# Performance work log

Measured on AMD Instinct MI355X. Metric: run time of the kernel, lower is better.

The kernel has to match this reference:

```python
import jax, jax.numpy as jnp
import numpy as np

N, DIN, E, BLK = 16384, 128, 262144, 2048
H1, DH1, H2, DH2 = 4, 128, 4, 128
D, L, HT, OUT = 128, 5, 4, 2


def _gat(h_in, src, dst, W, a_s, a_d, b, concat):
    # PyG GATConv (eval mode, no dropout): message src->dst, softmax per dst
    H, Dh = a_s.shape
    h = (h_in @ W).reshape(N, H, Dh)
    als = jnp.einsum('nhd,hd->nh', h, a_s)
    ald = jnp.einsum('nhd,hd->nh', h, a_d)
    e = jax.nn.leaky_relu(als[src] + ald[dst], 0.2)            # [E2,H]
    m = jax.ops.segment_max(e, dst, num_segments=N)
    ex = jnp.exp(e - m[dst])
    den = jax.ops.segment_sum(ex, dst, num_segments=N)
    alpha = ex / (den[dst] + 1e-16)
    out = jax.ops.segment_sum(alpha[:, :, None] * h[src], dst, num_segments=N)
    return (out.reshape(N, H * Dh) if concat else out.mean(axis=1)) + b


def _pe():
    pos = jnp.arange(L, dtype=jnp.float32)[:, None]
    div = jnp.exp(jnp.arange(0, D, 2, dtype=jnp.float32) * (-jnp.log(10000.0) / D))
    return jnp.zeros((L, D)).at[:, 0::2].set(jnp.sin(pos * div)).at[:, 1::2].set(jnp.cos(pos * div))


def reference(x, edge_index, time_step, W1, a_src1, a_dst1, b1, W2, a_src2, a_dst2, b2,
              wq, bq, wk, bk, wv, bv, wo, bo, ln_g, ln_b, f1, fb1, f2, fb2, wc, bc):
    s, d = edge_index[0], edge_index[1]
    loops = jnp.arange(N, dtype=edge_index.dtype)
    src = jnp.concatenate([s, d, loops])
    dst = jnp.concatenate([d, s, loops])

    # structural encoder (two GAT layers)
    h = jax.nn.elu(_gat(x, src, dst, W1, a_src1, a_dst1, b1, True))
    h2 = _gat(h, src, dst, W2, a_src2, a_dst2, b2, False)       # [N, D]

    # temporal self-attention: banks are empty (one snapshot per node), so
    # seq has only the last slot valid; original detaches seq before temporal.
    seq = jnp.zeros((N, L, D), h2.dtype).at[:, L - 1].set(jax.lax.stop_gradient(h2))
    xs = seq + _pe()[None]                                       # [N,L,D]
    dh = D // HT
    q = xs[:, -1]                                                # only last query is used
    Q = (q @ wq + bq).reshape(N, HT, dh)
    K = (xs @ wk + bk).reshape(N, L, HT, dh)
    V = (xs @ wv + bv).reshape(N, L, HT, dh)
    scores = jnp.einsum('nhd,nlhd->nhl', Q, K) / jnp.sqrt(jnp.float32(dh))
    valid = (jnp.arange(L) == L - 1)                             # key_padding_mask: pad except last
    scores = jnp.where(valid[None, None, :], scores, -1e9)
    attn = jax.nn.softmax(scores, axis=-1)
    ctx = jnp.einsum('nhl,nlhd->nhd', attn, V).reshape(N, D)
    ao = ctx @ wo + bo

    def ln(v):
        mu = v.mean(-1, keepdims=True)
        var = v.var(-1, keepdims=True)
        return (v - mu) / jnp.sqrt(var + 1e-5) * ln_g + ln_b

    y = ln(q + ao)
    y = ln(y + jax.nn.relu(y @ f1 + fb1) @ f2 + fb2)
    return y @ wc + bc                                           # [N, 2]


def setup_inputs():
    key = jax.random.key(0)
    ks = jax.random.split(key, 20)
    src = jax.random.randint(ks[0], (E,), 0, N, dtype=jnp.int32)
    off = jax.random.randint(ks[1], (E,), 0, BLK, dtype=jnp.int32)
    dst = (src // BLK) * BLK + off                               # within-snapshot edges
    r = lambda k, shape, s=0.05: jax.random.normal(k, shape, jnp.float32) * s
    return {
        'x': jax.random.normal(ks[2], (N, DIN), jnp.float32),
        'edge_index': jnp.stack([src, dst]),
        'time_step': (jnp.arange(N) // BLK).astype(jnp.int64),
        'W1': r(ks[3], (DIN, H1 * DH1)), 'a_src1': r(ks[4], (H1, DH1)), 'a_dst1': r(ks[5], (H1, DH1)), 'b1': jnp.zeros((H1 * DH1,)),
        'W2': r(ks[6], (H1 * DH1, H2 * DH2)), 'a_src2': r(ks[7], (H2, DH2)), 'a_dst2': r(ks[8], (H2, DH2)), 'b2': jnp.zeros((DH2,)),
        'wq': r(ks[9], (D, D)), 'bq': jnp.zeros((D,)), 'wk': r(ks[10], (D, D)), 'bk': jnp.zeros((D,)),
        'wv': r(ks[11], (D, D)), 'bv': jnp.zeros((D,)), 'wo': r(ks[12], (D, D)), 'bo': jnp.zeros((D,)),
        'ln_g': jnp.ones((D,)), 'ln_b': jnp.zeros((D,)),
        'f1': r(ks[13], (D, 4 * D)), 'fb1': jnp.zeros((4 * D,)), 'f2': r(ks[14], (4 * D, D)), 'fb2': jnp.zeros((D,)),
        'wc': r(ks[15], (D, OUT)), 'bc': jnp.zeros((OUT,)),
    }
```

## Files before the change

kernel.cpp:

```cpp
#include <hip/hip_runtime.h>
#include <hip/hip_bf16.h>

#define NODES 16384
#define FEAT 512
typedef __hip_bfloat16 bf16;
typedef __hip_bfloat162 bf162;
typedef short short8v __attribute__((ext_vector_type(8)));
typedef unsigned int uint4v __attribute__((ext_vector_type(4)));
typedef float f32x4 __attribute__((ext_vector_type(4)));

static __device__ __forceinline__ float b2f(short s){
  return __uint_as_float(((unsigned)(unsigned short)s) << 16);
}
static __device__ __forceinline__ void split_store(bf16* h, bf16* l, size_t i, float v){
  bf16 hi = __float2bfloat16(v);
  h[i] = hi; l[i] = __float2bfloat16(v - __bfloat162float(hi));
}

__global__ void sentinel_kernel(float* __restrict__ out, int n, float v){
  int i = blockIdx.x*blockDim.x + threadIdx.x;
  if (i < n) out[i] = v;
}

__global__ void zero_kernel(int* __restrict__ p, int n){
  int i = blockIdx.x*blockDim.x + threadIdx.x;
  if (i < n) p[i] = 0;
}
__global__ void count_kernel(const int* __restrict__ ei, int* __restrict__ counts, int E){
  int i = blockIdx.x*blockDim.x + threadIdx.x;
  if (i < 2*E){
    int dst = (i < E) ? ei[E+i] : ei[i-E];
    atomicAdd(&counts[dst], 1);
  }
}
__global__ __launch_bounds__(1024) void scan_kernel(const int* __restrict__ counts,
                                                    int* __restrict__ offs, int* __restrict__ cursor){
  __shared__ int sh[1024];
  const int t = threadIdx.x;
  int loc[16]; int s = 0;
#pragma unroll
  for (int i=0;i<16;i++){ loc[i] = counts[t*16+i]; s += loc[i]; }
  sh[t] = s; __syncthreads();
  for (int d=1; d<1024; d<<=1){
    int v = (t>=d) ? sh[t-d] : 0;
    __syncthreads(); sh[t] += v; __syncthreads();
  }
  int run = (t==0) ? 0 : sh[t-1];
#pragma unroll
  for (int i=0;i<16;i++){ offs[t*16+i] = run; cursor[t*16+i] = run; run += loc[i]; }
  if (t==1023) offs[NODES] = run;
}
__global__ void fill_kernel(const int* __restrict__ ei, int* __restrict__ cursor,
                            unsigned short* __restrict__ csr, int E){
  int i = blockIdx.x*blockDim.x + threadIdx.x;
  if (i < 2*E){
    int src = ei[i];
    int dst = (i < E) ? ei[E+i] : ei[i-E];
    int pos = atomicAdd(&cursor[dst], 1);
    csr[pos] = (unsigned short)src;
  }
}

struct PrepArgs {
  const float *x,*W1,*W2,*wv,*wo,*f1,*f2;
  bf16 *xh,*w1h,*w2h,*wvh,*wvl,*woh,*wol,*f1h,*f1l,*f2h,*f2l;
};
__global__ __launch_bounds__(256) void prep_kernel(PrepArgs P){
  const int b = blockIdx.x;
  const int t = threadIdx.x;
  if (b < 512){
    const size_t base = (size_t)b*4096;
#pragma unroll
    for (int k=0;k<16;k++){
      const size_t i = base + t + 256*k;
      P.xh[i] = __float2bfloat16(P.x[i]);
    }
    return;
  }
  __shared__ float tile[64][65];
  const float* src; bf16 *dh; bf16 *dl; int R, C, ti;
  int bb = b - 512;
  if (bb < 16){ src=P.W1; dh=P.w1h; dl=nullptr; R=128; C=512; ti=bb; }
  else if ((bb-=16) < 64){ src=P.W2; dh=P.w2h; dl=nullptr; R=512; C=512; ti=bb; }
  else if ((bb-=64) < 4){ src=P.wv; dh=P.wvh; dl=P.wvl; R=128; C=128; ti=bb; }
  else if ((bb-=4) < 4){ src=P.wo; dh=P.woh; dl=P.wol; R=128; C=128; ti=bb; }
  else if ((bb-=4) < 16){ src=P.f1; dh=P.f1h; dl=P.f1l; R=128; C=512; ti=bb; }
  else { bb-=16; src=P.f2; dh=P.f2h; dl=P.f2l; R=512; C=128; ti=bb; }
  const int ctiles = C/64;
  const int r0 = (ti/ctiles)*64, c0 = (ti%ctiles)*64;
  const int r = t >> 6, c = t & 63;
#pragma unroll
  for (int i=0;i<16;i++)
    tile[r + 4*i][c] = src[(size_t)(r0 + r + 4*i)*C + c0 + c];
  __syncthreads();
#pragma unroll
  for (int i=0;i<16;i++){
    const int oc   = c0 + r + 4*i;
    const int orow = r0 + c;
    const float v = tile[c][r + 4*i];
    const size_t oi = (size_t)oc*R + orow;
    if (dl){ split_store(dh, dl, oi, v); } else { dh[oi] = __float2bfloat16(v); }
  }
}

static __device__ __forceinline__ short8v ld8(const bf16* p){
  return *(const short8v*)(const void*)(p);
}

template<int K, int SA, int SB, int ACT, int OMODE, int ALS, int LNM>
__global__ __launch_bounds__(256) void lgemm(
    const bf16* __restrict__ A, const bf16* __restrict__ Al,
    const bf16* __restrict__ B, const bf16* __restrict__ Bl,
    const float* __restrict__ bias,
    float* __restrict__ Cf, bf16* __restrict__ Ch, bf16* __restrict__ Cl, int N,
    const float* __restrict__ as_p, const float* __restrict__ ad_p,
    float* __restrict__ als_p, float* __restrict__ ald_p,
    const float* __restrict__ qbuf, const float* __restrict__ lng, const float* __restrict__ lnb,
    float* __restrict__ y1f, bf16* __restrict__ y1ho, bf16* __restrict__ y1lo,
    const float* __restrict__ wcp, const float* __restrict__ bcp, float* __restrict__ outp){
  __shared__ bf16 As[128*40];
  __shared__ bf16 Bs[128*40];
  __shared__ bf16 Asl[SA ? 128*40 : 1];
  __shared__ bf16 Bsl[SB ? 128*40 : 1];
  const int tid = threadIdx.x;
  const int l = tid & 63, w = tid >> 6;
  const int lg = l >> 4, lr = l & 15;
  const int wr = w >> 1, wc = w & 1;
  const int r0 = blockIdx.x*128;
  const int c0 = blockIdx.y*128;
  const int srow = tid >> 1;
  const int spos = (tid & 1) * 16;
  f32x4 acc[4][4] = {};
  const int ard[4] = { (wr*64 +  0 + lr)*40 + lg*8, (wr*64 + 16 + lr)*40 + lg*8,
                       (wr*64 + 32 + lr)*40 + lg*8, (wr*64 + 48 + lr)*40 + lg*8 };
  const int brd[4] = { (wc*64 +  0 + lr)*40 + lg*8, (wc*64 + 16 + lr)*40 + lg*8,
                       (wc*64 + 32 + lr)*40 + lg*8, (wc*64 + 48 + lr)*40 + lg*8 };
  const size_t agbase = (size_t)(r0 + srow)*K + spos;
  const size_t bgbase = (size_t)(c0 + srow)*K + spos;
  const int sl = srow*40 + spos;
#pragma unroll
  for (int k0 = 0; k0 < K; k0 += 32){
    *(short8v*)&As[sl]     = ld8(A + agbase + k0);
    *(short8v*)&As[sl + 8] = ld8(A + agbase + k0 + 8);
    *(short8v*)&Bs[sl]     = ld8(B + bgbase + k0);
    *(short8v*)&Bs[sl + 8] = ld8(B + bgbase + k0 + 8);
    if (SA){
      *(short8v*)&Asl[sl]     = ld8(Al + agbase + k0);
      *(short8v*)&Asl[sl + 8] = ld8(Al + agbase + k0 + 8);
    }
    if (SB){
      *(short8v*)&Bsl[sl]     = ld8(Bl + bgbase + k0);
      *(short8v*)&Bsl[sl + 8] = ld8(Bl + bgbase + k0 + 8);
    }
    __syncthreads();
    short8v af[4], bfr[4], afl[4], bfl[4];
#pragma unroll
    for (int f=0; f<4; f++){
      af[f]  = *(const short8v*)&As[ard[f]];
      bfr[f] = *(const short8v*)&Bs[brd[f]];
      if (SA) afl[f] = *(const short8v*)&Asl[ard[f]];
      if (SB) bfl[f] = *(const short8v*)&Bsl[brd[f]];
    }
#pragma unroll
    for (int fm=0; fm<4; fm++)
#pragma unroll
      for (int fn=0; fn<4; fn++){
        acc[fm][fn] = __builtin_amdgcn_mfma_f32_16x16x32_bf16(af[fm], bfr[fn], acc[fm][fn], 0,0,0);
        if (SB) acc[fm][fn] = __builtin_amdgcn_mfma_f32_16x16x32_bf16(af[fm], bfl[fn], acc[fm][fn], 0,0,0);
        if (SA) acc[fm][fn] = __builtin_amdgcn_mfma_f32_16x16x32_bf16(afl[fm], bfr[fn], acc[fm][fn], 0,0,0);
      }
    __syncthreads();
  }
  if (LNM == 0){
    float asv[4], adv[4];
    float rs[4][4], rd[4][4];
    if (ALS){
#pragma unroll
      for (int fn=0; fn<4; fn++){
        const int col = c0 + wc*64 + fn*16 + lr;
        asv[fn] = as_p[col]; adv[fn] = ad_p[col];
      }
#pragma unroll
      for (int fm=0; fm<4; fm++)
#pragma unroll
        for (int r=0; r<4; r++){ rs[fm][r] = 0.f; rd[fm][r] = 0.f; }
    }
#pragma unroll
    for (int fm=0; fm<4; fm++){
#pragma unroll
      for (int fn=0; fn<4; fn++){
        const int col = c0 + wc*64 + fn*16 + lr;
        const float bv = bias ? bias[col] : 0.f;
#pragma unroll
        for (int r=0; r<4; r++){
          const int row = r0 + wr*64 + fm*16 + lg*4 + r;
          float v = acc[fm][fn][r] + bv;
          if (ACT==1) v = fmaxf(v, 0.f);
          const size_t idx = (size_t)row*N + col;
          if (OMODE==0) Cf[idx] = v;
          else if (OMODE==1){
            bf16 bvv = __float2bfloat16(v);
            Ch[idx] = bvv;
            if (ALS){
              const float hv = __bfloat162float(bvv);
              rs[fm][r] += hv*asv[fn];
              rd[fm][r] += hv*adv[fn];
            }
          }
          else split_store(Ch, Cl, idx, v);
        }
      }
    }
    if (ALS){
      float* rb = (float*)As;
#pragma unroll
      for (int fm=0; fm<4; fm++)
#pragma unroll
        for (int r=0; r<4; r++){
          float s = rs[fm][r], dd = rd[fm][r];
#pragma unroll
          for (int mask=1; mask<16; mask<<=1){
            s  += __shfl_xor(s,  mask);
            dd += __shfl_xor(dd, mask);
          }
          rs[fm][r] = s; rd[fm][r] = dd;
        }
      if (wc == 1 && lr == 0){
#pragma unroll
        for (int fm=0; fm<4; fm++)
#pragma unroll
          for (int r=0; r<4; r++){
            const int row = wr*64 + fm*16 + lg*4 + r;
            rb[row] = rs[fm][r]; rb[128+row] = rd[fm][r];
          }
      }
      __syncthreads();
      if (wc == 0 && lr == 0){
        const int head = blockIdx.y;
#pragma unroll
        for (int fm=0; fm<4; fm++)
#pragma unroll
          for (int r=0; r<4; r++){
            const int row = wr*64 + fm*16 + lg*4 + r;
            als_p[(size_t)(r0+row)*4 + head] = rs[fm][r] + rb[row];
            ald_p[(size_t)(r0+row)*4 + head] = rd[fm][r] + rb[128+row];
          }
      }
    }
  } else {
    float s1[4][4], s2[4][4];
#pragma unroll
    for (int fm=0; fm<4; fm++)
#pragma unroll
      for (int r=0; r<4; r++){ s1[fm][r] = 0.f; s2[fm][r] = 0.f; }
#pragma unroll
    for (int fm=0; fm<4; fm++)
#pragma unroll
      for (int fn=0; fn<4; fn++){
        const int col = wc*64 + fn*16 + lr;
        const float bv = bias[col];
#pragma unroll
        for (int r=0; r<4; r++){
          const int row = r0 + wr*64 + fm*16 + lg*4 + r;
          float xx = qbuf[(size_t)row*128 + col] + acc[fm][fn][r] + bv;
          acc[fm][fn][r] = xx;
          s1[fm][r] += xx;
          s2[fm][r] += xx*xx;
        }
      }
    float* rb = (float*)As;
#pragma unroll
    for (int fm=0; fm<4; fm++)
#pragma unroll
      for (int r=0; r<4; r++){
        float a = s1[fm][r], b = s2[fm][r];
#pragma unroll
        for (int mask=1; mask<16; mask<<=1){
          a += __shfl_xor(a, mask);
          b += __shfl_xor(b, mask);
        }
        s1[fm][r] = a; s2[fm][r] = b;
      }
    if (lr == 0){
#pragma unroll
      for (int fm=0; fm<4; fm++)
#pragma unroll
        for (int r=0; r<4; r++){
          const int row = wr*64 + fm*16 + lg*4 + r;
          rb[row*4 + wc*2 + 0] = s1[fm][r];
          rb[row*4 + wc*2 + 1] = s2[fm][r];
        }
    }
    __syncthreads();
    float mu[4][4], ri[4][4];
#pragma unroll
    for (int fm=0; fm<4; fm++)
#pragma unroll
      for (int r=0; r<4; r++){
        const int row = wr*64 + fm*16 + lg*4 + r;
        const float st  = s1[fm][r] + rb[row*4 + (wc^1)*2 + 0];
        const float s2t = s2[fm][r] + rb[row*4 + (wc^1)*2 + 1];
        const float m  = st*(1.f/128.f);
        const float va = s2t*(1.f/128.f) - m*m;
        mu[fm][r] = m;
        ri[fm][r] = 1.f/sqrtf(va + 1e-5f);
      }
    if (LNM == 1){
#pragma unroll
      for (int fm=0; fm<4; fm++)
#pragma unroll
        for (int fn=0; fn<4; fn++){
          const int col = wc*64 + fn*16 + lr;
          const float gv = lng[col], bbv = lnb[col];
#pragma unroll
          for (int r=0; r<4; r++){
            const int row = r0 + wr*64 + fm*16 + lg*4 + r;
            const float ln = (acc[fm][fn][r] - mu[fm][r])*ri[fm][r]*gv + bbv;
            const size_t idx = (size_t)row*128 + col;
            y1f[idx] = ln;
            split_store(y1ho, y1lo, idx, ln);
          }
        }
    } else {
      float p0[4][4], p1[4][4];
#pragma unroll
      for (int fm=0; fm<4; fm++)
#pragma unroll
        for (int r=0; r<4; r++){ p0[fm][r] = 0.f; p1[fm][r] = 0.f; }
#pragma unroll
      for (int fm=0; fm<4; fm++)
#pragma unroll
        for (int fn=0; fn<4; fn++){
          const int col = wc*64 + fn*16 + lr;
          const float gv = lng[col], bbv = lnb[col];
          const float w0 = wcp[col*2], w1 = wcp[col*2+1];
#pragma unroll
          for (int r=0; r<4; r++){
            const float ln = (acc[fm][fn][r] - mu[fm][r])*ri[fm][r]*gv + bbv;
            p0[fm][r] += ln*w0;
            p1[fm][r] += ln*w1;
          }
        }
      __syncthreads();
#pragma unroll
      for (int fm=0; fm<4; fm++)
#pragma unroll
        for (int r=0; r<4; r++){
          float a = p0[fm][r], b = p1[fm][r];
#pragma unroll
          for (int mask=1; mask<16; mask<<=1){
            a += __shfl_xor(a, mask);
            b += __shfl_xor(b, mask);
          }
          p0[fm][r] = a; p1[fm][r] = b;
        }
      if (lr == 0){
#pragma unroll
        for (int fm=0; fm<4; fm++)
#pragma unroll
          for (int r=0; r<4; r++){
            const int row = wr*64 + fm*16 + lg*4 + r;
            rb[row*4 + wc*2 + 0] = p0[fm][r];
            rb[row*4 + wc*2 + 1] = p1[fm][r];
          }
      }
      __syncthreads();
      if (wc == 0 && lr == 0){
#pragma unroll
        for (int fm=0; fm<4; fm++)
#pragma unroll
          for (int r=0; r<4; r++){
            const int row = wr*64 + fm*16 + lg*4 + r;
            outp[(size_t)(r0+row)*2 + 0] = p0[fm][r] + rb[row*4 + 2] + bcp[0];
            outp[(size_t)(r0+row)*2 + 1] = p1[fm][r] + rb[row*4 + 3] + bcp[1];
          }
      }
    }
  }
}

template<bool CONCAT>
__global__ __launch_bounds__(256) void gat_fused_kernel(const bf16* __restrict__ hfeat,
    const float* __restrict__ als, const float* __restrict__ ald,
    const int* __restrict__ offs, const unsigned short* __restrict__ csr,
    const float* __restrict__ bias, void* __restrict__ outv,
    bf16* __restrict__ qh, bf16* __restrict__ ql){
  const int w = threadIdx.x >> 6, l = threadIdx.x & 63, g = l >> 4, s16 = l & 15;
  const int nb = blockIdx.x;
  const int n = (nb & 7)*2048 + (nb >> 3)*4 + w;
  const float adg = ald[(size_t)n*4 + g];
  const int beg = offs[n];
  const int cnt = offs[n+1] - beg + 1;
  float ev[6]; int sv[6];
#pragma unroll
  for (int p=0;p<6;p++){
    const int i = s16 + p*16;
    int src = n;
    float e = -1e30f;
    if (i < cnt){
      if (i < cnt-1) src = (int)csr[beg+i];
      float t = als[(size_t)src*4+g] + adg;
      e = fmaxf(t, 0.2f*t);
    }
    ev[p] = e; sv[p] = src;
  }
  float m = -1e30f;
#pragma unroll
  for (int p=0;p<6;p++) m = fmaxf(m, ev[p]);
  float den = 0.f;
#pragma unroll
  for (int p=0;p<6;p++) den += (ev[p] > -1e29f) ? __expf(ev[p]-m) : 0.f;
#pragma unroll
  for (int mask=1; mask<16; mask<<=1){
    float mo = __shfl_xor(m, mask);
    float dd = __shfl_xor(den, mask);
    float nm = fmaxf(m, mo);
    den = den*__expf(m-nm) + dd*__expf(mo-nm);
    m = nm;
  }
  const float C = __expf(-m)/(den + 1e-16f);
  int pk[6];
#pragma unroll
  for (int p=0;p<6;p++){
    float a = (ev[p] > -1e29f) ? __expf(ev[p])*C : 0.f;
    bf16 ab = __float2bfloat16(a);
    pk[p] = ((int)*(unsigned short*)&ab << 16) | (sv[p] & 0xFFFF);
  }
  float acc[8] = {0,0,0,0,0,0,0,0};
  const int fb = l*8;
  const bf16* hp = hfeat + fb;
#pragma unroll
  for (int p=0;p<6;p++){
    const int pbase = p*16;
    if (pbase < cnt){
      const int lim = (cnt - pbase < 16) ? (cnt - pbase) : 16;
      int u_c = __shfl(pk[p], (l & 48));
      uint4v hv_c = *(const uint4v*)(const void*)(hp + (size_t)(u_c & 0xFFFF)*FEAT);
      for (int j=1; j<lim; ++j){
        const int u_n = __shfl(pk[p], (l & 48) | j);
        const uint4v hv_n = *(const uint4v*)(const void*)(hp + (size_t)(u_n & 0xFFFF)*FEAT);
        const float a_c = __uint_as_float((unsigned)u_c & 0xFFFF0000u);
#pragma unroll
        for (int k=0;k<4;k++){
          acc[2*k]   += a_c * __uint_as_float(hv_c[k] << 16);
          acc[2*k+1] += a_c * __uint_as_float(hv_c[k] & 0xFFFF0000u);
        }
        u_c = u_n; hv_c = hv_n;
      }
      const float a_c = __uint_as_float((unsigned)u_c & 0xFFFF0000u);
#pragma unroll
      for (int k=0;k<4;k++){
        acc[2*k]   += a_c * __uint_as_float(hv_c[k] << 16);
        acc[2*k+1] += a_c * __uint_as_float(hv_c[k] & 0xFFFF0000u);
      }
    }
  }
  for (int i = 96; i < cnt; ++i){
    const int src = (i < cnt-1) ? (int)csr[beg+i] : n;
    float t = als[(size_t)src*4+g] + adg;
    t = fmaxf(t, 0.2f*t);
    const float a = __expf(t)*C;
    const short8v hv = *(const short8v*)(const void*)&hfeat[(size_t)src*FEAT + fb];
#pragma unroll
    for (int k=0;k<8;k++) acc[k] += a * b2f(hv[k]);
  }
  if (CONCAT){
    short8v ov;
#pragma unroll
    for (int j=0;j<8;j++){
      float v = acc[j] + bias[fb+j];
      v = v > 0.f ? v : expm1f(v);
      bf16 bv = __float2bfloat16(v);
      ov[j] = (short)*(unsigned short*)&bv;
    }
    *(short8v*)((char*)outv + ((size_t)n*FEAT + fb)*2) = ov;
  } else {
#pragma unroll
    for (int j=0;j<8;j++){
      acc[j] += __shfl_xor(acc[j], 16);
      acc[j] += __shfl_xor(acc[j], 32);
    }
    if (l < 16){
      float* op = (float*)outv + (size_t)n*128 + l*8;
#pragma unroll
      for (int j=0;j<8;j++){
        const int col = l*8 + j;
        float v = 0.25f*acc[j] + bias[col];
        float ex = __expf((float)(col & ~1) * (-9.210340371976184f/128.f));
        float pe = (col & 1) ? cosf(4.f*ex) : sinf(4.f*ex);
        float q = v + pe;
        op[j] = q;
        split_store(qh, ql, (size_t)n*128 + col, q);
      }
    }
  }
}

extern "C" void kernel_launch(void* const* d_in, const int* in_sizes, int n_in,
                              void* d_out, int out_size, void* d_ws, size_t ws_size,
                              hipStream_t stream){
  const float* x      = (const float*)d_in[0];
  const int*   ei     = (const int*)d_in[1];
  const float* W1     = (const float*)d_in[3];
  const float* a_src1 = (const float*)d_in[4];
  const float* a_dst1 = (const float*)d_in[5];
  const float* b1     = (const float*)d_in[6];
  const float* W2     = (const float*)d_in[7];
  const float* a_src2 = (const float*)d_in[8];
  const float* a_dst2 = (const float*)d_in[9];
  const float* b2     = (const float*)d_in[10];
  const float* wv     = (const float*)d_in[15];
  const float* bv     = (const float*)d_in[16];
  const float* wo     = (const float*)d_in[17];
  const float* bo     = (const float*)d_in[18];
  const float* ln_g   = (const float*)d_in[19];
  const float* ln_b   = (const float*)d_in[20];
  const float* f1     = (const float*)d_in[21];
  const float* fb1    = (const float*)d_in[22];
  const float* f2     = (const float*)d_in[23];
  const float* fb2    = (const float*)d_in[24];
  const float* wc     = (const float*)d_in[25];
  const float* bc     = (const float*)d_in[26];
  float* outp = (float*)d_out;

  const int E = in_sizes[1] / 2;
  const int n = NODES;
  const int tE = 2*E;
  const size_t MB = 1024*1024;

  const size_t NEED = 36*MB;
  if (ws_size < NEED){
    sentinel_kernel<<<(out_size+255)/256, 256, 0, stream>>>(outp, out_size,
        1000.0f + (float)(ws_size / MB));
    return;
  }

  char* base = (char*)d_ws;
  int* counts = (int*)(base + 0);
  int* cursor = (int*)(base + 65536);
  bf16*  h1    = (bf16*)(base + 0);
  bf16*  xh    = (bf16*)(base + 16*MB);
  bf16*  h     = (bf16*)(base + 16*MB);
  bf16*  h2f   = (bf16*)(base + 0);
  float* h2q   = (float*)(base + 16*MB);
  bf16*  qh    = (bf16*)(base + 24*MB);
  bf16*  ql    = (bf16*)(base + 28*MB);
  bf16*  vh    = (bf16*)(base + 0);
  bf16*  vl    = (bf16*)(base + 4*MB);
  float* y1    = (float*)(base + 24*MB);
  bf16*  y1h   = (bf16*)(base + 0);
  bf16*  y1l   = (bf16*)(base + 4*MB);
  bf16*  hidden= (bf16*)(base + 8*MB);
  char* u = base + 32*MB;
  bf16* w1h = (bf16*)u; u += 131072;
  bf16* w2h = (bf16*)u; u += 524288;
  bf16* wvh = (bf16*)u; u += 32768;   bf16* wvl = (bf16*)u; u += 32768;
  bf16* woh = (bf16*)u; u += 32768;   bf16* wol = (bf16*)u; u += 32768;
  bf16* f1h = (bf16*)u; u += 131072;  bf16* f1l = (bf16*)u; u += 131072;
  bf16* f2h = (bf16*)u; u += 131072;  bf16* f2l = (bf16*)u; u += 131072;
  float* als  = (float*)u; u += (size_t)n*4*4;
  float* ald  = (float*)u; u += (size_t)n*4*4;
  int* offs   = (int*)u;   u += (size_t)(n+1)*4 + 252;
  unsigned short* csr = (unsigned short*)u; u += (size_t)tE*2;

  PrepArgs P = { x,W1,W2,wv,wo,f1,f2, xh,w1h,w2h,wvh,wvl,woh,wol,f1h,f1l,f2h,f2l };
  prep_kernel<<<632, 256, 0, stream>>>(P);
  zero_kernel<<<(n+255)/256, 256, 0, stream>>>(counts, n);
  count_kernel<<<(tE+255)/256, 256, 0, stream>>>(ei, counts, E);
  scan_kernel<<<1, 1024, 0, stream>>>(counts, offs, cursor);
  fill_kernel<<<(tE+255)/256, 256, 0, stream>>>(ei, cursor, csr, E);

  lgemm<128,0,0,0,1,1,0><<<dim3(128,4), 256, 0, stream>>>(xh, nullptr, w1h, nullptr, nullptr,
      nullptr, h1, nullptr, 512, a_src1, a_dst1, als, ald,
      nullptr,nullptr,nullptr,nullptr,nullptr,nullptr,nullptr,nullptr,nullptr);
  gat_fused_kernel<true><<<n/4, 256, 0, stream>>>(h1, als, ald, offs, csr, b1, h, nullptr, nullptr);

  lgemm<512,0,0,0,1,1,0><<<dim3(128,4), 256, 0, stream>>>(h, nullptr, w2h, nullptr, nullptr,
      nullptr, h2f, nullptr, 512, a_src2, a_dst2, als, ald,
      nullptr,nullptr,nullptr,nullptr,nullptr,nullptr,nullptr,nullptr,nullptr);
  gat_fused_kernel<false><<<n/4, 256, 0, stream>>>(h2f, als, ald, offs, csr, b2, h2q, qh, ql);

  lgemm<128,1,1,0,2,0,0><<<dim3(128,1), 256, 0, stream>>>(qh, ql, wvh, wvl, bv,
      nullptr, vh, vl, 128, nullptr, nullptr, nullptr, nullptr,
      nullptr,nullptr,nullptr,nullptr,nullptr,nullptr,nullptr,nullptr,nullptr);
  lgemm<128,1,1,0,0,0,1><<<dim3(128,1), 256, 0, stream>>>(vh, vl, woh, wol, bo,
      nullptr, nullptr, nullptr, 128, nullptr, nullptr, nullptr, nullptr,
      h2q, ln_g, ln_b, y1, y1h, y1l, nullptr, nullptr, nullptr);
  lgemm<128,1,1,1,1,0,0><<<dim3(128,4), 256, 0, stream>>>(y1h, y1l, f1h, f1l, fb1,
      nullptr, hidden, nullptr, 512, nullptr, nullptr, nullptr, nullptr,
      nullptr,nullptr,nullptr,nullptr,nullptr,nullptr,nullptr,nullptr,nullptr);
  lgemm<512,0,1,0,0,0,2><<<dim3(128,1), 256, 0, stream>>>(hidden, nullptr, f2h, f2l, fb2,
      nullptr, nullptr, nullptr, 128, nullptr, nullptr, nullptr, nullptr,
      y1, ln_g, ln_b, nullptr, nullptr, nullptr, wc, bc, outp);
}
```

Before: 252.9 us.

## Fuse V and O projections with LayerNorm into one attention chain kernel

Replaces the two back-to-back split-precision GEMM launches (V projection, then O projection with residual and LayerNorm) with a single kernel. That kernel keeps the V result in shared memory as hi/lo bf16 and feeds it straight into the O projection, so the vh/vl round trip through global memory and one launch go away. The LNM==1 branch is dropped from lgemm and workspace buffers are remapped. Separately, the GAT gather loop now prefetches two rows ahead instead of one to hide more load latency, at the cost of extra registers.

```diff
diff --git a/kernel.cpp b/kernel.cpp
--- a/kernel.cpp
+++ b/kernel.cpp
@@ -305,78 +305,234 @@
         mu[fm][r] = m;
         ri[fm][r] = 1.f/sqrtf(va + 1e-5f);
       }
-    if (LNM == 1){
+    float p0[4][4], p1[4][4];
+#pragma unroll
+    for (int fm=0; fm<4; fm++)
+#pragma unroll
+      for (int r=0; r<4; r++){ p0[fm][r] = 0.f; p1[fm][r] = 0.f; }
+#pragma unroll
+    for (int fm=0; fm<4; fm++)
+#pragma unroll
+      for (int fn=0; fn<4; fn++){
+        const int col = wc*64 + fn*16 + lr;
+        const float gv = lng[col], bbv = lnb[col];
+        const float w0 = wcp[col*2], w1 = wcp[col*2+1];
+#pragma unroll
+        for (int r=0; r<4; r++){
+          const float ln = (acc[fm][fn][r] - mu[fm][r])*ri[fm][r]*gv + bbv;
+          p0[fm][r] += ln*w0;
+          p1[fm][r] += ln*w1;
+        }
+      }
+    __syncthreads();
+#pragma unroll
+    for (int fm=0; fm<4; fm++)
+#pragma unroll
+      for (int r=0; r<4; r++){
+        float a = p0[fm][r], b = p1[fm][r];
+#pragma unroll
+        for (int mask=1; mask<16; mask<<=1){
+          a += __shfl_xor(a, mask);
+          b += __shfl_xor(b, mask);
+        }
+        p0[fm][r] = a; p1[fm][r] = b;
+      }
+    if (lr == 0){
 #pragma unroll
       for (int fm=0; fm<4; fm++)
 #pragma unroll
+        for (int r=0; r<4; r++){
+          const int row = wr*64 + fm*16 + lg*4 + r;
+          rb[row*4 + wc*2 + 0] = p0[fm][r];
+          rb[row*4 + wc*2 + 1] = p1[fm][r];
+        }
+    }
+    __syncthreads();
+    if (wc == 0 && lr == 0){
+#pragma unroll
+      for (int fm=0; fm<4; fm++)
+#pragma unroll
+        for (int r=0; r<4; r++){
+          const int row = wr*64 + fm*16 + lg*4 + r;
+          outp[(size_t)(r0+row)*2 + 0] = p0[fm][r] + rb[row*4 + 2] + bcp[0];
+          outp[(size_t)(r0+row)*2 + 1] = p1[fm][r] + rb[row*4 + 3] + bcp[1];
+        }
+    }
+  }
+}
+
+__global__ __launch_bounds__(256) void attn_chain_kernel(
+    const bf16* __restrict__ qh, const bf16* __restrict__ ql,
+    const bf16* __restrict__ wvh, const bf16* __restrict__ wvl,
+    const float* __restrict__ bv,
+    const bf16* __restrict__ woh, const bf16* __restrict__ wol,
+    const float* __restrict__ bo,
+    const float* __restrict__ h2q, const float* __restrict__ lng, const float* __restrict__ lnb,
+    float* __restrict__ y1f, bf16* __restrict__ y1ho, bf16* __restrict__ y1lo){
+  __shared__ bf16 As[128*40];
+  __shared__ bf16 Bs[128*40];
+  __shared__ bf16 Asl[128*40];
+  __shared__ bf16 Bsl[128*40];
+  const int tid = threadIdx.x;
+  const int l = tid & 63, w = tid >> 6;
+  const int lg = l >> 4, lr = l & 15;
+  const int wr = w >> 1, wc = w & 1;
+  const int r0 = blockIdx.x*128;
+  const int srow = tid >> 1;
+  const int spos = (tid & 1) * 16;
+  const int sl = srow*40 + spos;
+  const int ard[4] = { (wr*64 +  0 + lr)*40 + lg*8, (wr*64 + 16 + lr)*40 + lg*8,
+                       (wr*64 + 32 + lr)*40 + lg*8, (wr*64 + 48 + lr)*40 + lg*8 };
+  const int brd[4] = { (wc*64 +  0 + lr)*40 + lg*8, (wc*64 + 16 + lr)*40 + lg*8,
+                       (wc*64 + 32 + lr)*40 + lg*8, (wc*64 + 48 + lr)*40 + lg*8 };
+  f32x4 acc[4][4] = {};
+  {
+    const size_t ag = (size_t)(r0 + srow)*128 + spos;
+    const size_t bg = (size_t)srow*128 + spos;
+#pragma unroll
+    for (int k0 = 0; k0 < 128; k0 += 32){
+      *(short8v*)&As[sl]      = ld8(qh + ag + k0);
+      *(short8v*)&As[sl + 8]  = ld8(qh + ag + k0 + 8);
+      *(short8v*)&Asl[sl]     = ld8(ql + ag + k0);
+      *(short8v*)&Asl[sl + 8] = ld8(ql + ag + k0 + 8);
+      *(short8v*)&Bs[sl]      = ld8(wvh + bg + k0);
+      *(short8v*)&Bs[sl + 8]  = ld8(wvh + bg + k0 + 8);
+      *(short8v*)&Bsl[sl]     = ld8(wvl + bg + k0);
+      *(short8v*)&Bsl[sl + 8] = ld8(wvl + bg + k0 + 8);
+      __syncthreads();
+      short8v af[4], bfr[4], afl[4], bfl[4];
+#pragma unroll
+      for (int f=0; f<4; f++){
+        af[f]  = *(const short8v*)&As[ard[f]];
+        bfr[f] = *(const short8v*)&Bs[brd[f]];
+        afl[f] = *(const short8v*)&Asl[ard[f]];
+        bfl[f] = *(const short8v*)&Bsl[brd[f]];
+      }
+#pragma unroll
+      for (int fm=0; fm<4; fm++)
+#pragma unroll
         for (int fn=0; fn<4; fn++){
-          const int col = wc*64 + fn*16 + lr;
-          const float gv = lng[col], bbv = lnb[col];
-#pragma unroll
-          for (int r=0; r<4; r++){
-            const int row = r0 + wr*64 + fm*16 + lg*4 + r;
-            const float ln = (acc[fm][fn][r] - mu[fm][r])*ri[fm][r]*gv + bbv;
-            const size_t idx = (size_t)row*128 + col;
-            y1f[idx] = ln;
-            split_store(y1ho, y1lo, idx, ln);
+          acc[fm][fn] = __builtin_amdgcn_mfma_f32_16x16x32_bf16(af[fm], bfr[fn], acc[fm][fn], 0,0,0);
+          acc[fm][fn] = __builtin_amdgcn_mfma_f32_16x16x32_bf16(af[fm], bfl[fn], acc[fm][fn], 0,0,0);
+          acc[fm][fn] = __builtin_amdgcn_mfma_f32_16x16x32_bf16(afl[fm], bfr[fn], acc[fm][fn], 0,0,0);
+        }
+      __syncthreads();
+    }
+  }
+  f32x4 acc2[4][4] = {};
+  {
+    const size_t bg = (size_t)srow*128 + spos;
+#pragma unroll
+    for (int kb=0; kb<4; ++kb){
+      if (wc == (kb >> 1)){
+        const int fnb = (kb & 1)*2;
+#pragma unroll
+        for (int fm=0; fm<4; fm++)
+#pragma unroll
+          for (int fi=0; fi<2; fi++){
+            const int fn = fnb + fi;
+            const int col = wc*64 + fn*16 + lr;
+            const float bvv = bv[col];
+            const int kk = col - kb*32;
+#pragma unroll
+            for (int r=0; r<4; r++){
+              const int row = wr*64 + fm*16 + lg*4 + r;
+              const float v = acc[fm][fn][r] + bvv;
+              const bf16 hi = __float2bfloat16(v);
+              const bf16 lo = __float2bfloat16(v - __bfloat162float(hi));
+              As[row*40 + kk]  = hi;
+              Asl[row*40 + kk] = lo;
+            }
           }
-        }
-    } else {
-      float p0[4][4], p1[4][4];
+      }
+      *(short8v*)&Bs[sl]      = ld8(woh + bg + kb*32);
+      *(short8v*)&Bs[sl + 8]  = ld8(woh + bg + kb*32 + 8);
+      *(short8v*)&Bsl[sl]     = ld8(wol + bg + kb*32);
+      *(short8v*)&Bsl[sl + 8] = ld8(wol + bg + kb*32 + 8);
+      __syncthreads();
+      short8v af[4], bfr[4], afl[4], bfl[4];
+#pragma unroll
+      for (int f=0; f<4; f++){
+        af[f]  = *(const short8v*)&As[ard[f] - 0];
+        bfr[f] = *(const short8v*)&Bs[brd[f]];
+        afl[f] = *(const short8v*)&Asl[ard[f] - 0];
+        bfl[f] = *(const short8v*)&Bsl[brd[f]];
+      }
 #pragma unroll
       for (int fm=0; fm<4; fm++)
 #pragma unroll
-        for (int r=0; r<4; r++){ p0[fm][r] = 0.f; p1[fm][r] = 0.f; }
-#pragma unroll
-      for (int fm=0; fm<4; fm++)
-#pragma unroll
         for (int fn=0; fn<4; fn++){
-          const int col = wc*64 + fn*16 + lr;
-          const float gv = lng[col], bbv = lnb[col];
-          const float w0 = wcp[col*2], w1 = wcp[col*2+1];
-#pragma unroll
-          for (int r=0; r<4; r++){
-            const float ln = (acc[fm][fn][r] - mu[fm][r])*ri[fm][r]*gv + bbv;
-            p0[fm][r] += ln*w0;
-            p1[fm][r] += ln*w1;
-          }
+          acc2[fm][fn] = __builtin_amdgcn_mfma_f32_16x16x32_bf16(af[fm], bfr[fn], acc2[fm][fn], 0,0,0);
+          acc2[fm][fn] = __builtin_amdgcn_mfma_f32_16x16x32_bf16(af[fm], bfl[fn], acc2[fm][fn], 0,0,0);
+          acc2[fm][fn] = __builtin_amdgcn_mfma_f32_16x16x32_bf16(afl[fm], bfr[fn], acc2[fm][fn], 0,0,0);
         }
       __syncthreads();
-#pragma unroll
-      for (int fm=0; fm<4; fm++)
-#pragma unroll
-        for (int r=0; r<4; r++){
-          float a = p0[fm][r], b = p1[fm][r];
-#pragma unroll
-          for (int mask=1; mask<16; mask<<=1){
-            a += __shfl_xor(a, mask);
-            b += __shfl_xor(b, mask);
-          }
-          p0[fm][r] = a; p1[fm][r] = b;
-        }
-      if (lr == 0){
-#pragma unroll
-        for (int fm=0; fm<4; fm++)
-#pragma unroll
-          for (int r=0; r<4; r++){
-            const int row = wr*64 + fm*16 + lg*4 + r;
-            rb[row*4 + wc*2 + 0] = p0[fm][r];
-            rb[row*4 + wc*2 + 1] = p1[fm][r];
-          }
-      }
-      __syncthreads();
-      if (wc == 0 && lr == 0){
-#pragma unroll
-        for (int fm=0; fm<4; fm++)
-#pragma unroll
-          for (int r=0; r<4; r++){
-            const int row = wr*64 + fm*16 + lg*4 + r;
-            outp[(size_t)(r0+row)*2 + 0] = p0[fm][r] + rb[row*4 + 2] + bcp[0];
-            outp[(size_t)(r0+row)*2 + 1] = p1[fm][r] + rb[row*4 + 3] + bcp[1];
-          }
-      }
-    }
-  }
+    }
+  }
+  float s1[4][4], s2[4][4];
+#pragma unroll
+  for (int fm=0; fm<4; fm++)
+#pragma unroll
+    for (int r=0; r<4; r++){ s1[fm][r] = 0.f; s2[fm][r] = 0.f; }
+#pragma unroll
+  for (int fm=0; fm<4; fm++)
+#pragma unroll
+    for (int fn=0; fn<4; fn++){
+      const int col = wc*64 + fn*16 + lr;
+      const float bvv = bo[col];
+#pragma unroll
+      for (int r=0; r<4; r++){
+        const int row = r0 + wr*64 + fm*16 + lg*4 + r;
+        float xx = h2q[(size_t)row*128 + col] + acc2[fm][fn][r] + bvv;
+        acc2[fm][fn][r] = xx;
+        s1[fm][r] += xx;
+        s2[fm][r] += xx*xx;
+      }
+    }
+  float* rb = (float*)As;
+#pragma unroll
+  for (int fm=0; fm<4; fm++)
+#pragma unroll
+    for (int r=0; r<4; r++){
+      float a = s1[fm][r], b = s2[fm][r];
+#pragma unroll
+      for (int mask=1; mask<16; mask<<=1){
+        a += __shfl_xor(a, mask);
+        b += __shfl_xor(b, mask);
+      }
+      s1[fm][r] = a; s2[fm][r] = b;
+    }
+  if (lr == 0){
+#pragma unroll
+    for (int fm=0; fm<4; fm++)
+#pragma unroll
+      for (int r=0; r<4; r++){
+        const int row = wr*64 + fm*16 + lg*4 + r;
+        rb[row*4 + wc*2 + 0] = s1[fm][r];
+        rb[row*4 + wc*2 + 1] = s2[fm][r];
+      }
+  }
+  __syncthreads();
+#pragma unroll
+  for (int fm=0; fm<4; fm++)
+#pragma unroll
+    for (int fn=0; fn<4; fn++){
+      const int col = wc*64 + fn*16 + lr;
+      const float gv = lng[col], bbv = lnb[col];
+#pragma unroll
+      for (int r=0; r<4; r++){
+        const int row4 = wr*64 + fm*16 + lg*4 + r;
+        const float st  = s1[fm][r] + rb[row4*4 + (wc^1)*2 + 0];
+        const float s2t = s2[fm][r] + rb[row4*4 + (wc^1)*2 + 1];
+        const float m  = st*(1.f/128.f);
+        const float va = s2t*(1.f/128.f) - m*m;
+        const float ri = 1.f/sqrtf(va + 1e-5f);
+        const float ln = (acc2[fm][fn][r] - m)*ri*gv + bbv;
+        const size_t idx = (size_t)(r0+row4)*128 + col;
+        y1f[idx] = ln;
+        split_store(y1ho, y1lo, idx, ln);
+      }
+    }
 }
 
 template<bool CONCAT>
@@ -429,32 +585,34 @@
   float acc[8] = {0,0,0,0,0,0,0,0};
   const int fb = l*8;
   const bf16* hp = hfeat + fb;
+#define PROC(U,H) { const float a_ = __uint_as_float((unsigned)(U) & 0xFFFF0000u); \
+  _Pragma("unroll") for (int k_=0;k_<4;k_++){ \
+    acc[2*k_]   += a_ * __uint_as_float((H)[k_] << 16); \
+    acc[2*k_+1] += a_ * __uint_as_float((H)[k_] & 0xFFFF0000u); } }
 #pragma unroll
   for (int p=0;p<6;p++){
     const int pbase = p*16;
     if (pbase < cnt){
       const int lim = (cnt - pbase < 16) ? (cnt - pbase) : 16;
-      int u_c = __shfl(pk[p], (l & 48));
-      uint4v hv_c = *(const uint4v*)(const void*)(hp + (size_t)(u_c & 0xFFFF)*FEAT);
-      for (int j=1; j<lim; ++j){
-        const int u_n = __shfl(pk[p], (l & 48) | j);
-        const uint4v hv_n = *(const uint4v*)(const void*)(hp + (size_t)(u_n & 0xFFFF)*FEAT);
-        const float a_c = __uint_as_float((unsigned)u_c & 0xFFFF0000u);
-#pragma unroll
-        for (int k=0;k<4;k++){
-          acc[2*k]   += a_c * __uint_as_float(hv_c[k] << 16);
-          acc[2*k+1] += a_c * __uint_as_float(hv_c[k] & 0xFFFF0000u);
-        }
-        u_c = u_n; hv_c = hv_n;
-      }
-      const float a_c = __uint_as_float((unsigned)u_c & 0xFFFF0000u);
-#pragma unroll
-      for (int k=0;k<4;k++){
-        acc[2*k]   += a_c * __uint_as_float(hv_c[k] << 16);
-        acc[2*k+1] += a_c * __uint_as_float(hv_c[k] & 0xFFFF0000u);
-      }
-    }
-  }
+      int u0 = __shfl(pk[p], (l & 48));
+      uint4v h0 = *(const uint4v*)(const void*)(hp + (size_t)(u0 & 0xFFFF)*FEAT);
+      if (lim == 1){
+        PROC(u0, h0);
+      } else {
+        int u1 = __shfl(pk[p], (l & 48) | 1);
+        uint4v h1 = *(const uint4v*)(const void*)(hp + (size_t)(u1 & 0xFFFF)*FEAT);
+        for (int j=2; j<lim; ++j){
+          const int u2 = __shfl(pk[p], (l & 48) | j);
+          const uint4v h2 = *(const uint4v*)(const void*)(hp + (size_t)(u2 & 0xFFFF)*FEAT);
+          PROC(u0, h0);
+          u0 = u1; h0 = h1; u1 = u2; h1 = h2;
+        }
+        PROC(u0, h0);
+        PROC(u1, h1);
+      }
+    }
+  }
+#undef PROC
   for (int i = 96; i < cnt; ++i){
     const int src = (i < cnt-1) ? (int)csr[beg+i] : n;
     float t = als[(size_t)src*4+g] + adg;
@@ -545,12 +703,10 @@
   float* h2q   = (float*)(base + 16*MB);
   bf16*  qh    = (bf16*)(base + 24*MB);
   bf16*  ql    = (bf16*)(base + 28*MB);
-  bf16*  vh    = (bf16*)(base + 0);
-  bf16*  vl    = (bf16*)(base + 4*MB);
-  float* y1    = (float*)(base + 24*MB);
   bf16*  y1h   = (bf16*)(base + 0);
   bf16*  y1l   = (bf16*)(base + 4*MB);
-  bf16*  hidden= (bf16*)(base + 8*MB);
+  float* y1f   = (float*)(base + 8*MB);
+  bf16*  hidden= (bf16*)(base + 16*MB);
   char* u = base + 32*MB;
   bf16* w1h = (bf16*)u; u += 131072;
   bf16* w2h = (bf16*)u; u += 524288;
@@ -580,16 +736,12 @@
       nullptr,nullptr,nullptr,nullptr,nullptr,nullptr,nullptr,nullptr,nullptr);
   gat_fused_kernel<false><<<n/4, 256, 0, stream>>>(h2f, als, ald, offs, csr, b2, h2q, qh, ql);
 
-  lgemm<128,1,1,0,2,0,0><<<dim3(128,1), 256, 0, stream>>>(qh, ql, wvh, wvl, bv,
-      nullptr, vh, vl, 128, nullptr, nullptr, nullptr, nullptr,
-      nullptr,nullptr,nullptr,nullptr,nullptr,nullptr,nullptr,nullptr,nullptr);
-  lgemm<128,1,1,0,0,0,1><<<dim3(128,1), 256, 0, stream>>>(vh, vl, woh, wol, bo,
-      nullptr, nullptr, nullptr, 128, nullptr, nullptr, nullptr, nullptr,
-      h2q, ln_g, ln_b, y1, y1h, y1l, nullptr, nullptr, nullptr);
+  attn_chain_kernel<<<128, 256, 0, stream>>>(qh, ql, wvh, wvl, bv, woh, wol, bo,
+      h2q, ln_g, ln_b, y1f, y1h, y1l);
   lgemm<128,1,1,1,1,0,0><<<dim3(128,4), 256, 0, stream>>>(y1h, y1l, f1h, f1l, fb1,
       nullptr, hidden, nullptr, 512, nullptr, nullptr, nullptr, nullptr,
       nullptr,nullptr,nullptr,nullptr,nullptr,nullptr,nullptr,nullptr,nullptr);
   lgemm<512,0,1,0,0,0,2><<<dim3(128,1), 256, 0, stream>>>(hidden, nullptr, f2h, f2l, fb2,
       nullptr, nullptr, nullptr, 128, nullptr, nullptr, nullptr, nullptr,
-      y1, ln_g, ln_b, nullptr, nullptr, nullptr, wc, bc, outp);
-}
+      y1f, ln_g, ln_b, nullptr, nullptr, nullptr, wc, bc, outp);
+}
```

Result: no change. 250.1 us (-1.1%).
